# Kernel optimization log

Measured on AMD Instinct MI355X. Metric: run time of the kernel, lower is better.

Reference implementation:

```python
import jax, jax.numpy as jnp
import numpy as np

B = 8192
N = 1024


def euler_to_matrix_xyz(e):
    # e: [B,3] angles; R = Rx(a) @ Ry(b) @ Rz(c) (pytorch3d 'XYZ' convention)
    a, b, c = e[..., 0], e[..., 1], e[..., 2]
    ca, sa = jnp.cos(a), jnp.sin(a)
    cb, sb = jnp.cos(b), jnp.sin(b)
    cc, sc = jnp.cos(c), jnp.sin(c)
    one = jnp.ones_like(a)
    zero = jnp.zeros_like(a)
    Rx = jnp.stack([one, zero, zero,
                    zero, ca, -sa,
                    zero, sa, ca], axis=-1).reshape(-1, 3, 3)
    Ry = jnp.stack([cb, zero, sb,
                    zero, one, zero,
                    -sb, zero, cb], axis=-1).reshape(-1, 3, 3)
    Rz = jnp.stack([cc, -sc, zero,
                    sc, cc, zero,
                    zero, zero, one], axis=-1).reshape(-1, 3, 3)
    return jnp.einsum('bij,bjk->bik', Rx, jnp.einsum('bij,bjk->bik', Ry, Rz))


def manifold2euler(manifold, mode):
    m1, m2, m3, m4 = (manifold[:, 0], manifold[:, 1], manifold[:, 2], manifold[:, 3])
    sgn = jnp.where(mode > 0.5, 1.0, -1.0)
    euler2 = sgn * jnp.arcsin(jnp.sqrt(m3 ** 2 / (m1 ** 2 + m2 ** 2 + m3 ** 2)))
    euler3 = jnp.arctan2(m4, m3 / (jnp.sin(euler2) + 1e-9))
    tmp = jnp.cos(euler2) * jnp.cos(euler3)
    euler1 = jnp.arctan2(m2 / tmp, m1 / tmp)
    euler3 = jnp.where(euler3 > 0, euler3, euler3 + 2 * np.pi)
    return jnp.stack([euler1, euler2, euler3], axis=-1)


def setup_inputs() -> dict:
    key = jax.random.key(0)
    k1, k2, k3, k4 = jax.random.split(key, 4)
    return {
        'pred': jax.random.normal(k1, (B, 4), dtype=jnp.float32),
        'mode': jax.random.uniform(k2, (B,), dtype=jnp.float32),
        'gt': jax.random.normal(k3, (B, 3), dtype=jnp.float32),
        'point': jax.random.normal(k4, (B, N, 3), dtype=jnp.float32),
    }


def reference(pred, mode, gt, point):
    euler_pred = manifold2euler(pred, mode)          # [B,3]
    rm_gt = euler_to_matrix_xyz(gt)                  # [B,3,3]
    rm_pred = euler_to_matrix_xyz(euler_pred)        # [B,3,3]
    # original: row-vector point [*,1,3] @ R [*,3,3]; R depends only on batch
    point_gt = jnp.einsum('bnj,bjk->bnk', point, rm_gt)
    point_pred = jnp.einsum('bnj,bjk->bnk', point, rm_pred)
    diff = point_pred - point_gt                     # [B,N,3]
    dist = jnp.linalg.norm(diff, axis=-1)            # [B,N]
    return jnp.mean(dist)
```

## Files before the change

### kernel.cpp

```cpp
#include <hip/hip_runtime.h>
#include <math.h>

constexpr int B_ = 8192;
constexpr int N_ = 1024;
constexpr int NTHREADS = 256;
constexpr float SCALE = 1.0f / ((float)B_ * (float)N_);

__device__ __forceinline__ void euler_to_mat(float a, float b, float c, float R[9]) {
    float ca = cosf(a), sa = sinf(a);
    float cb = cosf(b), sb = sinf(b);
    float cc = cosf(c), sc = sinf(c);
    R[0] = cb * cc;                R[1] = -cb * sc;               R[2] = sb;
    R[3] = ca * sc + sa * sb * cc; R[4] = ca * cc - sa * sb * sc; R[5] = -sa * cb;
    R[6] = sa * sc - ca * sb * cc; R[7] = sa * cc + ca * sb * sc; R[8] = ca * cb;
}

__device__ __forceinline__ void compute_M(const float* __restrict__ pred,
                                          const float* __restrict__ mode,
                                          const float* __restrict__ gt,
                                          int b, float M[9]) {
    float m1 = pred[b * 4 + 0], m2 = pred[b * 4 + 1];
    float m3 = pred[b * 4 + 2], m4 = pred[b * 4 + 3];
    float sgn = (mode[b] > 0.5f) ? 1.0f : -1.0f;
    float e2 = sgn * asinf(sqrtf(m3 * m3 / (m1 * m1 + m2 * m2 + m3 * m3)));
    float e3 = atan2f(m4, m3 / (sinf(e2) + 1e-9f));
    float tmp = cosf(e2) * cosf(e3);
    float e1 = atan2f(m2 / tmp, m1 / tmp);
    e3 = (e3 > 0.0f) ? e3 : (e3 + 6.2831854820251465f);
    float P[9], G[9];
    euler_to_mat(e1, e2, e3, P);
    euler_to_mat(gt[b * 3 + 0], gt[b * 3 + 1], gt[b * 3 + 2], G);
    #pragma unroll
    for (int i = 0; i < 9; ++i) M[i] = P[i] - G[i];
}

__global__ __launch_bounds__(256)
void prep_M_kernel(const float* __restrict__ pred, const float* __restrict__ mode,
                   const float* __restrict__ gt, float* __restrict__ Mout) {
    int b = blockIdx.x * blockDim.x + threadIdx.x;
    if (b >= B_) return;
    float M[9];
    compute_M(pred, mode, gt, b, M);
    #pragma unroll
    for (int i = 0; i < 9; ++i) Mout[b * 9 + i] = M[i];
}

__device__ __forceinline__ float dist3(float px, float py, float pz, const float M[9]) {
    float dx = px * M[0] + py * M[3] + pz * M[6];
    float dy = px * M[1] + py * M[4] + pz * M[7];
    float dz = px * M[2] + py * M[5] + pz * M[8];
    return sqrtf(dx * dx + dy * dy + dz * dz);
}

__global__ __launch_bounds__(NTHREADS)
void point_kernel(const float* __restrict__ point,
                  const float* __restrict__ Mg,
                  float* __restrict__ partial)
{
    const int b = blockIdx.x;
    const int t = threadIdx.x;
    __shared__ float sM[9];
    __shared__ float swave[NTHREADS / 64];

    if (t < 9) sM[t] = Mg[b * 9 + t];
    __syncthreads();
    float M[9];
    #pragma unroll
    for (int i = 0; i < 9; ++i) M[i] = sM[i];

    const float4* gp = (const float4*)(point + (size_t)b * (N_ * 3));
    float4 p0 = gp[3 * t + 0];
    float4 p1 = gp[3 * t + 1];
    float4 p2 = gp[3 * t + 2];

    float local = dist3(p0.x, p0.y, p0.z, M)
                + dist3(p0.w, p1.x, p1.y, M)
                + dist3(p1.z, p1.w, p2.x, M)
                + dist3(p2.y, p2.z, p2.w, M);

    #pragma unroll
    for (int off = 32; off > 0; off >>= 1)
        local += __shfl_down(local, off, 64);
    if ((t & 63) == 0) swave[t >> 6] = local;
    __syncthreads();
    if (t == 0) partial[b] = swave[0] + swave[1] + swave[2] + swave[3];
}

__global__ __launch_bounds__(1024)
void reduce_kernel(const float* __restrict__ partial, float* __restrict__ out) {
    __shared__ float swave[1024 / 64];
    const int t = threadIdx.x;
    float local = 0.0f;
    #pragma unroll
    for (int i = 0; i < B_ / 1024; ++i) local += partial[t + 1024 * i];
    #pragma unroll
    for (int off = 32; off > 0; off >>= 1)
        local += __shfl_down(local, off, 64);
    if ((t & 63) == 0) swave[t >> 6] = local;
    __syncthreads();
    if (t == 0) {
        float s = 0.0f;
        #pragma unroll
        for (int i = 0; i < 1024 / 64; ++i) s += swave[i];
        out[0] = s * SCALE;
    }
}

__global__ __launch_bounds__(NTHREADS)
void fused_kernel(const float* __restrict__ pred, const float* __restrict__ mode,
                  const float* __restrict__ gt, const float* __restrict__ point,
                  float* __restrict__ out) {
    const int b = blockIdx.x;
    const int t = threadIdx.x;
    __shared__ float swave[NTHREADS / 64];
    float M[9];
    compute_M(pred, mode, gt, b, M);
    const float4* gp = (const float4*)(point + (size_t)b * (N_ * 3));
    float4 p0 = gp[3 * t + 0];
    float4 p1 = gp[3 * t + 1];
    float4 p2 = gp[3 * t + 2];
    float local = dist3(p0.x, p0.y, p0.z, M)
                + dist3(p0.w, p1.x, p1.y, M)
                + dist3(p1.z, p1.w, p2.x, M)
                + dist3(p2.y, p2.z, p2.w, M);
    #pragma unroll
    for (int off = 32; off > 0; off >>= 1)
        local += __shfl_down(local, off, 64);
    if ((t & 63) == 0) swave[t >> 6] = local;
    __syncthreads();
    if (t == 0)
        atomicAdd(out, (swave[0] + swave[1] + swave[2] + swave[3]) * SCALE);
}

extern "C" void kernel_launch(void* const* d_in, const int* in_sizes, int n_in,
                              void* d_out, int out_size, void* d_ws, size_t ws_size,
                              hipStream_t stream) {
    const float* pred  = (const float*)d_in[0];
    const float* mode  = (const float*)d_in[1];
    const float* gt    = (const float*)d_in[2];
    const float* point = (const float*)d_in[3];
    float* out = (float*)d_out;

    const size_t need = (size_t)(B_ * 9 + B_) * sizeof(float);
    if (ws_size >= need) {
        float* Mg      = (float*)d_ws;
        float* partial = Mg + B_ * 9;
        prep_M_kernel<<<B_ / 256, 256, 0, stream>>>(pred, mode, gt, Mg);
        point_kernel<<<B_, NTHREADS, 0, stream>>>(point, Mg, partial);
        reduce_kernel<<<1, 1024, 0, stream>>>(partial, out);
    } else {
        hipMemsetAsync(out, 0, sizeof(float), stream);
        fused_kernel<<<B_, NTHREADS, 0, stream>>>(pred, mode, gt, point, out);
    }
}
```

Before: 153.8 us.

## Fuse rotation prep into point kernel with one wave per batch

Drops the separate prep_M kernel. Each wave now computes its batch's rotation difference matrix itself, overlapped with issuing twelve nontemporal float4 loads per lane. Mapping one batch per wave removes the shared-memory block reduction and the __syncthreads, and also cuts one kernel launch. In exchange, the transcendental math is done redundantly by all 64 lanes of the wave, and more registers are used to hold the prefetched points.

New measurement: 152.7 us. Within noise of the previous version (-0.7%).

```diff
diff --git a/kernel.cpp b/kernel.cpp
--- a/kernel.cpp
+++ b/kernel.cpp
@@ -4,7 +4,11 @@
 constexpr int B_ = 8192;
 constexpr int N_ = 1024;
 constexpr int NTHREADS = 256;
+constexpr int WPB = NTHREADS / 64;
+constexpr int NBLOCKS = B_ / WPB;
 constexpr float SCALE = 1.0f / ((float)B_ * (float)N_);
+
+typedef float vfloat4 __attribute__((ext_vector_type(4)));
 
 __device__ __forceinline__ void euler_to_mat(float a, float b, float c, float R[9]) {
     float ca = cosf(a), sa = sinf(a);
@@ -34,18 +38,7 @@
     for (int i = 0; i < 9; ++i) M[i] = P[i] - G[i];
 }
 
-__global__ __launch_bounds__(256)
-void prep_M_kernel(const float* __restrict__ pred, const float* __restrict__ mode,
-                   const float* __restrict__ gt, float* __restrict__ Mout) {
-    int b = blockIdx.x * blockDim.x + threadIdx.x;
-    if (b >= B_) return;
-    float M[9];
-    compute_M(pred, mode, gt, b, M);
-    #pragma unroll
-    for (int i = 0; i < 9; ++i) Mout[b * 9 + i] = M[i];
-}
-
-__device__ __forceinline__ float dist3(float px, float py, float pz, const float M[9]) {
+__device__ __forceinline__ float dist3(float px, float py, float pz, const float* M) {
     float dx = px * M[0] + py * M[3] + pz * M[6];
     float dy = px * M[1] + py * M[4] + pz * M[7];
     float dz = px * M[2] + py * M[5] + pz * M[8];
@@ -53,37 +46,39 @@
 }
 
 __global__ __launch_bounds__(NTHREADS)
-void point_kernel(const float* __restrict__ point,
-                  const float* __restrict__ Mg,
-                  float* __restrict__ partial)
+void fused_main(const float* __restrict__ pred, const float* __restrict__ mode,
+                const float* __restrict__ gt, const float* __restrict__ point,
+                float* __restrict__ partial)
 {
-    const int b = blockIdx.x;
-    const int t = threadIdx.x;
-    __shared__ float sM[9];
-    __shared__ float swave[NTHREADS / 64];
+    const int wave = threadIdx.x >> 6;
+    const int lane = threadIdx.x & 63;
+    const int b    = blockIdx.x * WPB + wave;
 
-    if (t < 9) sM[t] = Mg[b * 9 + t];
-    __syncthreads();
+    const vfloat4* gp4 = (const vfloat4*)(point + (size_t)b * (N_ * 3));
+    vfloat4 P[4][3];
+    #pragma unroll
+    for (int j = 0; j < 4; ++j)
+        #pragma unroll
+        for (int k = 0; k < 3; ++k)
+            P[j][k] = __builtin_nontemporal_load(&gp4[192 * j + 3 * lane + k]);
+
     float M[9];
+    compute_M(pred, mode, gt, b, M);
+
+    float local = 0.0f;
     #pragma unroll
-    for (int i = 0; i < 9; ++i) M[i] = sM[i];
-
-    const float4* gp = (const float4*)(point + (size_t)b * (N_ * 3));
-    float4 p0 = gp[3 * t + 0];
-    float4 p1 = gp[3 * t + 1];
-    float4 p2 = gp[3 * t + 2];
-
-    float local = dist3(p0.x, p0.y, p0.z, M)
-                + dist3(p0.w, p1.x, p1.y, M)
-                + dist3(p1.z, p1.w, p2.x, M)
-                + dist3(p2.y, p2.z, p2.w, M);
+    for (int j = 0; j < 4; ++j) {
+        const vfloat4 p0 = P[j][0], p1 = P[j][1], p2 = P[j][2];
+        local += dist3(p0.x, p0.y, p0.z, M)
+               + dist3(p0.w, p1.x, p1.y, M)
+               + dist3(p1.z, p1.w, p2.x, M)
+               + dist3(p2.y, p2.z, p2.w, M);
+    }
 
     #pragma unroll
     for (int off = 32; off > 0; off >>= 1)
         local += __shfl_down(local, off, 64);
-    if ((t & 63) == 0) swave[t >> 6] = local;
-    __syncthreads();
-    if (t == 0) partial[b] = swave[0] + swave[1] + swave[2] + swave[3];
+    if (lane == 0) partial[b] = local;
 }
 
 __global__ __launch_bounds__(1024)
@@ -107,29 +102,34 @@
 }
 
 __global__ __launch_bounds__(NTHREADS)
-void fused_kernel(const float* __restrict__ pred, const float* __restrict__ mode,
+void fused_atomic(const float* __restrict__ pred, const float* __restrict__ mode,
                   const float* __restrict__ gt, const float* __restrict__ point,
                   float* __restrict__ out) {
-    const int b = blockIdx.x;
-    const int t = threadIdx.x;
-    __shared__ float swave[NTHREADS / 64];
+    const int wave = threadIdx.x >> 6;
+    const int lane = threadIdx.x & 63;
+    const int b    = blockIdx.x * WPB + wave;
+    const vfloat4* gp4 = (const vfloat4*)(point + (size_t)b * (N_ * 3));
+    vfloat4 P[4][3];
+    #pragma unroll
+    for (int j = 0; j < 4; ++j)
+        #pragma unroll
+        for (int k = 0; k < 3; ++k)
+            P[j][k] = __builtin_nontemporal_load(&gp4[192 * j + 3 * lane + k]);
     float M[9];
     compute_M(pred, mode, gt, b, M);
-    const float4* gp = (const float4*)(point + (size_t)b * (N_ * 3));
-    float4 p0 = gp[3 * t + 0];
-    float4 p1 = gp[3 * t + 1];
-    float4 p2 = gp[3 * t + 2];
-    float local = dist3(p0.x, p0.y, p0.z, M)
-                + dist3(p0.w, p1.x, p1.y, M)
-                + dist3(p1.z, p1.w, p2.x, M)
-                + dist3(p2.y, p2.z, p2.w, M);
+    float local = 0.0f;
+    #pragma unroll
+    for (int j = 0; j < 4; ++j) {
+        const vfloat4 p0 = P[j][0], p1 = P[j][1], p2 = P[j][2];
+        local += dist3(p0.x, p0.y, p0.z, M)
+               + dist3(p0.w, p1.x, p1.y, M)
+               + dist3(p1.z, p1.w, p2.x, M)
+               + dist3(p2.y, p2.z, p2.w, M);
+    }
     #pragma unroll
     for (int off = 32; off > 0; off >>= 1)
         local += __shfl_down(local, off, 64);
-    if ((t & 63) == 0) swave[t >> 6] = local;
-    __syncthreads();
-    if (t == 0)
-        atomicAdd(out, (swave[0] + swave[1] + swave[2] + swave[3]) * SCALE);
+    if (lane == 0) atomicAdd(out, local * SCALE);
 }
 
 extern "C" void kernel_launch(void* const* d_in, const int* in_sizes, int n_in,
@@ -141,15 +141,12 @@
     const float* point = (const float*)d_in[3];
     float* out = (float*)d_out;
 
-    const size_t need = (size_t)(B_ * 9 + B_) * sizeof(float);
-    if (ws_size >= need) {
-        float* Mg      = (float*)d_ws;
-        float* partial = Mg + B_ * 9;
-        prep_M_kernel<<<B_ / 256, 256, 0, stream>>>(pred, mode, gt, Mg);
-        point_kernel<<<B_, NTHREADS, 0, stream>>>(point, Mg, partial);
+    if (ws_size >= (size_t)B_ * sizeof(float)) {
+        float* partial = (float*)d_ws;
+        fused_main<<<NBLOCKS, NTHREADS, 0, stream>>>(pred, mode, gt, point, partial);
         reduce_kernel<<<1, 1024, 0, stream>>>(partial, out);
     } else {
-        hipMemsetAsync(out, 0, sizeof(float), stream);
-        fused_kernel<<<B_, NTHREADS, 0, stream>>>(pred, mode, gt, point, out);
+        (void)hipMemsetAsync(out, 0, sizeof(float), stream);
+        fused_atomic<<<NBLOCKS, NTHREADS, 0, stream>>>(pred, mode, gt, point, out);
     }
 }
```
